# Performance work log

Hardware: AMD Instinct MI355X
Metric: run time of the kernel (lower is better)

Reference implementation:

```python
import jax, jax.numpy as jnp
import numpy as np

WEIGHT = 1.0  # init kwarg 'weight'


def _histc(x, bins):
    """torch.histc semantics: bins over [x.min(), x.max()], rightmost bin inclusive."""
    mn, mx = x.min(), x.max()
    w = (mx - mn) / bins
    safe_w = jnp.where(w > 0, w, 1.0)
    b = jnp.clip(jnp.floor((x - mn) / safe_w), 0, bins - 1).astype(jnp.int32)
    return jnp.zeros((bins,), jnp.float32).at[b].add(1.0)


def setup_inputs() -> dict:
    key = jax.random.key(0)
    k1, k2, k3 = jax.random.split(key, 3)
    C, H, W = 64, 128, 128
    inp = jax.random.normal(k1, (1, C, H, W), jnp.float32)
    match = jax.random.normal(k2, (1, C, H, W), jnp.float32)
    mask_tight = (jax.random.uniform(k3, (1, 1, H, W)) > 0.3).astype(jnp.float32)
    return {"input": inp, "match": match, "mask_tight": mask_tight, "bins": 256}


def reference(input, match, mask_tight, bins):
    C = input.shape[1]
    # --- compute_histogram (torch.histc per channel of masked match) ---
    mm = (match * mask_tight).reshape(C, -1)
    style_his = jax.lax.stop_gradient(jax.vmap(lambda v: _histc(v, bins))(mm))  # (C, bins)

    # --- remap_histogram ---
    x = (input * mask_tight).reshape(C, -1)  # (C, N)
    N = x.shape[1]
    channel_min = x.min(1, keepdims=True)  # (C,1)
    channel_max = x.max(1, keepdims=True)  # (C,1)
    step = (channel_max - channel_min) / bins
    rng = jnp.arange(1, N + 1, dtype=x.dtype)[None, :]  # (1, N) ranks 1..N

    sh = style_his * N / style_his.sum(1, keepdims=True)
    cdf = jnp.cumsum(sh, axis=1)                                  # (C, bins)
    cdf_prev = jnp.concatenate([jnp.zeros((C, 1), cdf.dtype), cdf[:, :-1]], axis=1)

    # CDF inversion: count bins whose cdf < rank  -> idx in [0, bins]
    idx = jnp.sum(cdf[:, None, :] - rng[:, :, None] < 0, axis=2).astype(jnp.int32)  # (C, N)

    # Faithful select_idx: gather from FLATTENED hist with un-offset bin indices
    flat_idx = idx.reshape(-1)
    sel = lambda h: h.reshape(-1)[flat_idx].reshape(C, N)

    ratio = jnp.clip((rng - sel(cdf_prev)) / (1e-8 + sel(cdf)), 0.0, 1.0)  # (C, N)
    input_corr = channel_min + (ratio + idx) * step
    input_corr = input_corr.at[:, -1].set(channel_max[:, 0])
    input_corr = sel(input_corr)  # faithful final flattened re-gather

    # --- loss (scalar stored as self.loss in the torch module) ---
    loss = jnp.mean((input_corr - x) ** 2)
    loss = loss * mask_tight.sum() * C / input.size * WEIGHT
    return loss
```

## Files before the change

kernel.cpp:

```cpp
#include <hip/hip_runtime.h>
#include <math.h>

#define C_CH   64
#define HW     16384
#define BINS   256
#define SPLIT  8
#define SEG    (HW / SPLIT)
#define NTHR   256

#define WS_ENC_MIN 0
#define WS_ENC_MAX 65
#define WS_SSE     130
#define WS_MASKSUM 131
#define WS_CDF     192
#define WS_T       (WS_CDF + C_CH * BINS)

__device__ inline unsigned int encf(float f) {
    unsigned int u = __float_as_uint(f);
    return (u & 0x80000000u) ? ~u : (u | 0x80000000u);
}
__device__ inline float decf(unsigned int e) {
    unsigned int u = (e & 0x80000000u) ? (e ^ 0x80000000u) : ~e;
    return __uint_as_float(u);
}

__global__ __launch_bounds__(NTHR) void k1_minmax(const float* __restrict__ input,
                                                  const float* __restrict__ match,
                                                  const float* __restrict__ mask,
                                                  unsigned int* __restrict__ ws) {
    const int c   = blockIdx.x >> 3;
    const int s   = blockIdx.x & (SPLIT - 1);
    const int tid = threadIdx.x;
    const int base = s * SEG;

    const float* m = match + c * HW + base;
    const float* mk = mask + base;

    float mn = INFINITY, mx = -INFINITY;
    #pragma unroll
    for (int k = 0; k < SEG / NTHR; k++) {
        float v = m[tid + k * NTHR] * mk[tid + k * NTHR];
        mn = fminf(mn, v);
        mx = fmaxf(mx, v);
    }

    __shared__ float red[NTHR];
    red[tid] = mn; __syncthreads();
    for (int st = 128; st > 0; st >>= 1) { if (tid < st) red[tid] = fminf(red[tid], red[tid + st]); __syncthreads(); }
    if (tid == 0) atomicMin(&ws[WS_ENC_MIN + c], encf(red[0]));
    __syncthreads();
    red[tid] = mx; __syncthreads();
    for (int st = 128; st > 0; st >>= 1) { if (tid < st) red[tid] = fmaxf(red[tid], red[tid + st]); __syncthreads(); }
    if (tid == 0) atomicMax(&ws[WS_ENC_MAX + c], encf(red[0]));

    if (c == 0) {
        const float* x = input + base;
        float xmn = INFINITY, xmx = -INFINITY, msum = 0.0f;
        #pragma unroll
        for (int k = 0; k < SEG / NTHR; k++) {
            float mv = mk[tid + k * NTHR];
            float v = x[tid + k * NTHR] * mv;
            xmn = fminf(xmn, v);
            xmx = fmaxf(xmx, v);
            msum += mv;
        }
        __syncthreads();
        red[tid] = xmn; __syncthreads();
        for (int st = 128; st > 0; st >>= 1) { if (tid < st) red[tid] = fminf(red[tid], red[tid + st]); __syncthreads(); }
        if (tid == 0) atomicMin(&ws[WS_ENC_MIN + C_CH], encf(red[0]));
        __syncthreads();
        red[tid] = xmx; __syncthreads();
        for (int st = 128; st > 0; st >>= 1) { if (tid < st) red[tid] = fmaxf(red[tid], red[tid + st]); __syncthreads(); }
        if (tid == 0) atomicMax(&ws[WS_ENC_MAX + C_CH], encf(red[0]));
        __syncthreads();
        red[tid] = msum; __syncthreads();
        for (int st = 128; st > 0; st >>= 1) { if (tid < st) red[tid] += red[tid + st]; __syncthreads(); }
        if (tid == 0) atomicAdd((float*)&ws[WS_MASKSUM], red[0]);
    }
}

__global__ __launch_bounds__(1024) void k2_hist(const float* __restrict__ match,
                                                const float* __restrict__ mask,
                                                unsigned int* __restrict__ ws) {
    const int c   = blockIdx.x;
    const int tid = threadIdx.x;
    const float* m = match + c * HW;
    float* wsf = (float*)ws;

    const float mn = decf(ws[WS_ENC_MIN + c]);
    const float mx = decf(ws[WS_ENC_MAX + c]);
    float w  = (mx - mn) * (1.0f / 256.0f);
    float sw = (w > 0.0f) ? w : 1.0f;

    __shared__ int hist[BINS];
    if (tid < BINS) hist[tid] = 0;
    __syncthreads();

    #pragma unroll
    for (int k = 0; k < HW / 1024; k++) {
        int i = tid + k * 1024;
        float v = m[i] * mask[i];
        float b = floorf((v - mn) / sw);
        b = fminf(fmaxf(b, 0.0f), 255.0f);
        atomicAdd(&hist[(int)b], 1);
    }
    __syncthreads();

    for (int off = 1; off < BINS; off <<= 1) {
        int v = 0;
        if (tid < BINS) v = hist[tid] + ((tid >= off) ? hist[tid - off] : 0);
        __syncthreads();
        if (tid < BINS) hist[tid] = v;
        __syncthreads();
    }

    if (tid < BINS) wsf[WS_CDF + c * BINS + tid] = (float)hist[tid];

    if (c == 0 && tid < BINS) {
        const float xmn = decf(ws[WS_ENC_MIN + C_CH]);
        const float xmx = decf(ws[WS_ENC_MAX + C_CH]);
        float step = (xmx - xmn) * (1.0f / 256.0f);
        float rank = (float)(tid + 1);
        int idx = 0;
        #pragma unroll 8
        for (int b = 0; b < BINS; b++) idx += (hist[b] < (tid + 1)) ? 1 : 0;
        float cp = (idx > 0) ? (float)hist[idx - 1] : 0.0f;
        float cc = (float)hist[idx];
        float ratio = (rank - cp) / (1e-8f + cc);
        ratio = fminf(fmaxf(ratio, 0.0f), 1.0f);
        wsf[WS_T + tid] = xmn + (ratio + (float)idx) * step;
    }
}

__global__ __launch_bounds__(NTHR) void k3_loss(const float* __restrict__ input,
                                                const float* __restrict__ mask,
                                                unsigned int* __restrict__ ws) {
    const int c   = blockIdx.x >> 3;
    const int s   = blockIdx.x & (SPLIT - 1);
    const int tid = threadIdx.x;
    const int base = s * SEG;
    const float* wsf = (const float*)ws;

    __shared__ float scdf[BINS];
    __shared__ float sT[BINS];
    if (tid < BINS) {
        scdf[tid] = wsf[WS_CDF + c * BINS + tid];
        sT[tid]   = wsf[WS_T + tid];
    }
    __syncthreads();

    const float* x  = input + c * HW + base;
    const float* mk = mask + base;

    int n0 = base + tid;
    float rank0 = (float)(n0 + 1);
    int lo = 0, hi = BINS;
    while (lo < hi) {
        int mid = (lo + hi) >> 1;
        if (scdf[mid] < rank0) lo = mid + 1; else hi = mid;
    }

    float acc = 0.0f;
    #pragma unroll
    for (int k = 0; k < SEG / NTHR; k++) {
        int i = tid + k * NTHR;
        float rank = (float)(base + i + 1);
        while (scdf[lo] < rank) lo++;
        float corr = sT[lo];
        float xv = x[i] * mk[i];
        float d = corr - xv;
        acc += d * d;
    }

    __shared__ float red[NTHR];
    red[tid] = acc; __syncthreads();
    for (int st = 128; st > 0; st >>= 1) { if (tid < st) red[tid] += red[tid + st]; __syncthreads(); }
    if (tid == 0) atomicAdd((float*)&ws[WS_SSE], red[0]);
}

__global__ void k4_final(const unsigned int* __restrict__ ws, float* __restrict__ out) {
    if (threadIdx.x == 0) {
        const float* wsf = (const float*)ws;
        double sse = (double)wsf[WS_SSE];
        double msum = (double)wsf[WS_MASKSUM];
        double mean = sse / (double)(C_CH * HW);
        out[0] = (float)(mean * msum * (double)C_CH / (double)(C_CH * HW));
    }
}

extern "C" void kernel_launch(void* const* d_in, const int* in_sizes, int n_in,
                              void* d_out, int out_size, void* d_ws, size_t ws_size,
                              hipStream_t stream) {
    const float* input = (const float*)d_in[0];
    const float* match = (const float*)d_in[1];
    const float* mask  = (const float*)d_in[2];
    unsigned int* ws   = (unsigned int*)d_ws;
    float* out         = (float*)d_out;

    hipMemsetAsync(ws + WS_ENC_MIN, 0xFF, 65 * sizeof(unsigned int), stream);
    hipMemsetAsync(ws + WS_ENC_MAX, 0x00, (132 - WS_ENC_MAX) * sizeof(unsigned int), stream);

    k1_minmax<<<C_CH * SPLIT, NTHR, 0, stream>>>(input, match, mask, ws);
    k2_hist  <<<C_CH, 1024, 0, stream>>>(match, mask, ws);
    k3_loss  <<<C_CH * SPLIT, NTHR, 0, stream>>>(input, mask, ws);
    k4_final <<<1, 64, 0, stream>>>(ws, out);
}
```

Measured before the change: 96.66 us.

## Fuse all stages into one cooperative kernel with grid syncs

Replaces the two memsets and four kernel launches with a single cooperative kernel that uses grid-wide syncs between the min/max, histogram, CDF/remap and loss phases. Per-block partials written to workspace replace the global atomics. The histogram is split across 8 blocks per channel, and loads are vectorized to float4. This removes launch and memset overhead and keeps more blocks busy during histogramming, at the cost of grid.sync latency and each block redundantly rescanning the channel-0 histogram.

```diff
diff --git a/kernel.cpp b/kernel.cpp
--- a/kernel.cpp
+++ b/kernel.cpp
@@ -1,5 +1,8 @@
 #include <hip/hip_runtime.h>
+#include <hip/hip_cooperative_groups.h>
 #include <math.h>
+
+namespace cg = cooperative_groups;
 
 #define C_CH   64
 #define HW     16384
@@ -7,184 +10,198 @@
 #define SPLIT  8
 #define SEG    (HW / SPLIT)
 #define NTHR   256
-
-#define WS_ENC_MIN 0
-#define WS_ENC_MAX 65
-#define WS_SSE     130
-#define WS_MASKSUM 131
-#define WS_CDF     192
-#define WS_T       (WS_CDF + C_CH * BINS)
-
-__device__ inline unsigned int encf(float f) {
-    unsigned int u = __float_as_uint(f);
-    return (u & 0x80000000u) ? ~u : (u | 0x80000000u);
-}
-__device__ inline float decf(unsigned int e) {
-    unsigned int u = (e & 0x80000000u) ? (e ^ 0x80000000u) : ~e;
-    return __uint_as_float(u);
-}
-
-__global__ __launch_bounds__(NTHR) void k1_minmax(const float* __restrict__ input,
-                                                  const float* __restrict__ match,
-                                                  const float* __restrict__ mask,
-                                                  unsigned int* __restrict__ ws) {
-    const int c   = blockIdx.x >> 3;
-    const int s   = blockIdx.x & (SPLIT - 1);
-    const int tid = threadIdx.x;
+#define NBLK   (C_CH * SPLIT)
+
+#define WS_PMN   0
+#define WS_PMX   512
+#define WS_PXMN  1024
+#define WS_PXMX  1032
+#define WS_PMS   1040
+#define WS_SSE   1048
+#define WS_HIST8 2048
+
+__device__ inline float4 ld4(const float* p) { return *(const float4*)p; }
+
+__device__ inline int lbound(const float* a, float rank) {
+    int lo = 0, hi = BINS;
+    while (lo < hi) { int mid = (lo + hi) >> 1; if (a[mid] < rank) lo = mid + 1; else hi = mid; }
+    return (lo > 255) ? 255 : lo;
+}
+
+__device__ inline void scan256(int* h, int tid) {
+    for (int off = 1; off < BINS; off <<= 1) {
+        int v = h[tid] + ((tid >= off) ? h[tid - off] : 0);
+        __syncthreads();
+        h[tid] = v;
+        __syncthreads();
+    }
+}
+
+__device__ inline float blk_reduce(float v, float* red, int tid, bool is_min, bool is_max) {
+    red[tid] = v; __syncthreads();
+    for (int st = 128; st > 0; st >>= 1) {
+        if (tid < st) {
+            float a = red[tid], b = red[tid + st];
+            red[tid] = is_min ? fminf(a, b) : (is_max ? fmaxf(a, b) : (a + b));
+        }
+        __syncthreads();
+    }
+    float r = red[0]; __syncthreads();
+    return r;
+}
+
+__global__ __launch_bounds__(NTHR, 2) void fused(const float* __restrict__ input,
+                                                 const float* __restrict__ match,
+                                                 const float* __restrict__ mask,
+                                                 float* ws, float* out) {
+    cg::grid_group grid = cg::this_grid();
+    const int b = blockIdx.x, c = b >> 3, s = b & (SPLIT - 1), tid = threadIdx.x;
     const int base = s * SEG;
-
-    const float* m = match + c * HW + base;
+    int* wsi = (int*)ws;
+
+    __shared__ float red[NTHR];
+    __shared__ int   ihist[BINS];
+    __shared__ float scdf[BINS];
+    __shared__ float sT[BINS];
+
+    const float* m  = match + c * HW + base;
     const float* mk = mask + base;
-
-    float mn = INFINITY, mx = -INFINITY;
-    #pragma unroll
-    for (int k = 0; k < SEG / NTHR; k++) {
-        float v = m[tid + k * NTHR] * mk[tid + k * NTHR];
-        mn = fminf(mn, v);
-        mx = fmaxf(mx, v);
-    }
-
-    __shared__ float red[NTHR];
-    red[tid] = mn; __syncthreads();
-    for (int st = 128; st > 0; st >>= 1) { if (tid < st) red[tid] = fminf(red[tid], red[tid + st]); __syncthreads(); }
-    if (tid == 0) atomicMin(&ws[WS_ENC_MIN + c], encf(red[0]));
-    __syncthreads();
-    red[tid] = mx; __syncthreads();
-    for (int st = 128; st > 0; st >>= 1) { if (tid < st) red[tid] = fmaxf(red[tid], red[tid + st]); __syncthreads(); }
-    if (tid == 0) atomicMax(&ws[WS_ENC_MAX + c], encf(red[0]));
-
-    if (c == 0) {
-        const float* x = input + base;
-        float xmn = INFINITY, xmx = -INFINITY, msum = 0.0f;
-        #pragma unroll
-        for (int k = 0; k < SEG / NTHR; k++) {
-            float mv = mk[tid + k * NTHR];
-            float v = x[tid + k * NTHR] * mv;
-            xmn = fminf(xmn, v);
-            xmx = fmaxf(xmx, v);
-            msum += mv;
-        }
-        __syncthreads();
-        red[tid] = xmn; __syncthreads();
-        for (int st = 128; st > 0; st >>= 1) { if (tid < st) red[tid] = fminf(red[tid], red[tid + st]); __syncthreads(); }
-        if (tid == 0) atomicMin(&ws[WS_ENC_MIN + C_CH], encf(red[0]));
-        __syncthreads();
-        red[tid] = xmx; __syncthreads();
-        for (int st = 128; st > 0; st >>= 1) { if (tid < st) red[tid] = fmaxf(red[tid], red[tid + st]); __syncthreads(); }
-        if (tid == 0) atomicMax(&ws[WS_ENC_MAX + C_CH], encf(red[0]));
-        __syncthreads();
-        red[tid] = msum; __syncthreads();
-        for (int st = 128; st > 0; st >>= 1) { if (tid < st) red[tid] += red[tid + st]; __syncthreads(); }
-        if (tid == 0) atomicAdd((float*)&ws[WS_MASKSUM], red[0]);
-    }
-}
-
-__global__ __launch_bounds__(1024) void k2_hist(const float* __restrict__ match,
-                                                const float* __restrict__ mask,
-                                                unsigned int* __restrict__ ws) {
-    const int c   = blockIdx.x;
-    const int tid = threadIdx.x;
-    const float* m = match + c * HW;
-    float* wsf = (float*)ws;
-
-    const float mn = decf(ws[WS_ENC_MIN + c]);
-    const float mx = decf(ws[WS_ENC_MAX + c]);
-    float w  = (mx - mn) * (1.0f / 256.0f);
-    float sw = (w > 0.0f) ? w : 1.0f;
-
-    __shared__ int hist[BINS];
-    if (tid < BINS) hist[tid] = 0;
-    __syncthreads();
-
-    #pragma unroll
-    for (int k = 0; k < HW / 1024; k++) {
-        int i = tid + k * 1024;
-        float v = m[i] * mask[i];
-        float b = floorf((v - mn) / sw);
-        b = fminf(fmaxf(b, 0.0f), 255.0f);
-        atomicAdd(&hist[(int)b], 1);
-    }
-    __syncthreads();
-
-    for (int off = 1; off < BINS; off <<= 1) {
-        int v = 0;
-        if (tid < BINS) v = hist[tid] + ((tid >= off) ? hist[tid - off] : 0);
-        __syncthreads();
-        if (tid < BINS) hist[tid] = v;
-        __syncthreads();
-    }
-
-    if (tid < BINS) wsf[WS_CDF + c * BINS + tid] = (float)hist[tid];
-
-    if (c == 0 && tid < BINS) {
-        const float xmn = decf(ws[WS_ENC_MIN + C_CH]);
-        const float xmx = decf(ws[WS_ENC_MAX + C_CH]);
+    const float* x  = input + c * HW + base;
+
+    {
+        float mn = INFINITY, mx = -INFINITY;
+        #pragma unroll
+        for (int k = 0; k < 2; k++) {
+            float4 mv = ld4(m + k * 1024 + 4 * tid);
+            float4 kv = ld4(mk + k * 1024 + 4 * tid);
+            float v0 = mv.x * kv.x, v1 = mv.y * kv.y, v2 = mv.z * kv.z, v3 = mv.w * kv.w;
+            mn = fminf(mn, fminf(fminf(v0, v1), fminf(v2, v3)));
+            mx = fmaxf(mx, fmaxf(fmaxf(v0, v1), fmaxf(v2, v3)));
+        }
+        mn = blk_reduce(mn, red, tid, true, false);
+        mx = blk_reduce(mx, red, tid, false, true);
+        if (tid == 0) { ws[WS_PMN + b] = mn; ws[WS_PMX + b] = mx; }
+
+        if (c == 0) {
+            float xmn = INFINITY, xmx = -INFINITY, msum = 0.0f;
+            #pragma unroll
+            for (int k = 0; k < 2; k++) {
+                float4 xv = ld4(x + k * 1024 + 4 * tid);
+                float4 kv = ld4(mk + k * 1024 + 4 * tid);
+                float v0 = xv.x * kv.x, v1 = xv.y * kv.y, v2 = xv.z * kv.z, v3 = xv.w * kv.w;
+                xmn = fminf(xmn, fminf(fminf(v0, v1), fminf(v2, v3)));
+                xmx = fmaxf(xmx, fmaxf(fmaxf(v0, v1), fmaxf(v2, v3)));
+                msum += kv.x + kv.y + kv.z + kv.w;
+            }
+            xmn = blk_reduce(xmn, red, tid, true, false);
+            xmx = blk_reduce(xmx, red, tid, false, true);
+            msum = blk_reduce(msum, red, tid, false, false);
+            if (tid == 0) { ws[WS_PXMN + s] = xmn; ws[WS_PXMX + s] = xmx; ws[WS_PMS + s] = msum; }
+        }
+    }
+    __threadfence();
+    grid.sync();
+
+    {
+        float mn = INFINITY, mx = -INFINITY;
+        #pragma unroll
+        for (int j = 0; j < SPLIT; j++) {
+            mn = fminf(mn, ws[WS_PMN + c * SPLIT + j]);
+            mx = fmaxf(mx, ws[WS_PMX + c * SPLIT + j]);
+        }
+        float w  = (mx - mn) * (1.0f / 256.0f);
+        float sw = (w > 0.0f) ? w : 1.0f;
+
+        ihist[tid] = 0;
+        __syncthreads();
+        #pragma unroll
+        for (int k = 0; k < 2; k++) {
+            float4 mv = ld4(m + k * 1024 + 4 * tid);
+            float4 kv = ld4(mk + k * 1024 + 4 * tid);
+            float v[4] = { mv.x * kv.x, mv.y * kv.y, mv.z * kv.z, mv.w * kv.w };
+            #pragma unroll
+            for (int j = 0; j < 4; j++) {
+                float bb = floorf((v[j] - mn) / sw);
+                bb = fminf(fmaxf(bb, 0.0f), 255.0f);
+                atomicAdd(&ihist[(int)bb], 1);
+            }
+        }
+        __syncthreads();
+        wsi[WS_HIST8 + b * BINS + tid] = ihist[tid];
+    }
+    __threadfence();
+    grid.sync();
+
+    {
+        int h = 0;
+        #pragma unroll
+        for (int j = 0; j < SPLIT; j++) h += wsi[WS_HIST8 + (c * SPLIT + j) * BINS + tid];
+        ihist[tid] = h;
+        __syncthreads();
+        scan256(ihist, tid);
+        scdf[tid] = (float)ihist[tid];
+        __syncthreads();
+
+        if (c != 0) {
+            int h0 = 0;
+            #pragma unroll
+            for (int j = 0; j < SPLIT; j++) h0 += wsi[WS_HIST8 + j * BINS + tid];
+            ihist[tid] = h0;
+            __syncthreads();
+            scan256(ihist, tid);
+        }
+        red[tid] = (float)ihist[tid];
+        __syncthreads();
+
+        float xmn = INFINITY, xmx = -INFINITY;
+        #pragma unroll
+        for (int j = 0; j < SPLIT; j++) {
+            xmn = fminf(xmn, ws[WS_PXMN + j]);
+            xmx = fmaxf(xmx, ws[WS_PXMX + j]);
+        }
         float step = (xmx - xmn) * (1.0f / 256.0f);
         float rank = (float)(tid + 1);
-        int idx = 0;
-        #pragma unroll 8
-        for (int b = 0; b < BINS; b++) idx += (hist[b] < (tid + 1)) ? 1 : 0;
-        float cp = (idx > 0) ? (float)hist[idx - 1] : 0.0f;
-        float cc = (float)hist[idx];
-        float ratio = (rank - cp) / (1e-8f + cc);
-        ratio = fminf(fmaxf(ratio, 0.0f), 1.0f);
-        wsf[WS_T + tid] = xmn + (ratio + (float)idx) * step;
-    }
-}
-
-__global__ __launch_bounds__(NTHR) void k3_loss(const float* __restrict__ input,
-                                                const float* __restrict__ mask,
-                                                unsigned int* __restrict__ ws) {
-    const int c   = blockIdx.x >> 3;
-    const int s   = blockIdx.x & (SPLIT - 1);
-    const int tid = threadIdx.x;
-    const int base = s * SEG;
-    const float* wsf = (const float*)ws;
-
-    __shared__ float scdf[BINS];
-    __shared__ float sT[BINS];
-    if (tid < BINS) {
-        scdf[tid] = wsf[WS_CDF + c * BINS + tid];
-        sT[tid]   = wsf[WS_T + tid];
-    }
-    __syncthreads();
-
-    const float* x  = input + c * HW + base;
-    const float* mk = mask + base;
-
-    int n0 = base + tid;
-    float rank0 = (float)(n0 + 1);
-    int lo = 0, hi = BINS;
-    while (lo < hi) {
-        int mid = (lo + hi) >> 1;
-        if (scdf[mid] < rank0) lo = mid + 1; else hi = mid;
-    }
-
-    float acc = 0.0f;
-    #pragma unroll
-    for (int k = 0; k < SEG / NTHR; k++) {
-        int i = tid + k * NTHR;
-        float rank = (float)(base + i + 1);
-        while (scdf[lo] < rank) lo++;
-        float corr = sT[lo];
-        float xv = x[i] * mk[i];
-        float d = corr - xv;
-        acc += d * d;
-    }
-
-    __shared__ float red[NTHR];
-    red[tid] = acc; __syncthreads();
-    for (int st = 128; st > 0; st >>= 1) { if (tid < st) red[tid] += red[tid + st]; __syncthreads(); }
-    if (tid == 0) atomicAdd((float*)&ws[WS_SSE], red[0]);
-}
-
-__global__ void k4_final(const unsigned int* __restrict__ ws, float* __restrict__ out) {
-    if (threadIdx.x == 0) {
-        const float* wsf = (const float*)ws;
-        double sse = (double)wsf[WS_SSE];
-        double msum = (double)wsf[WS_MASKSUM];
-        double mean = sse / (double)(C_CH * HW);
-        out[0] = (float)(mean * msum * (double)C_CH / (double)(C_CH * HW));
+        int idx = lbound(red, rank);
+        float cp = (idx > 0) ? red[idx - 1] : 0.0f;
+        float cc = red[idx];
+        float ratio = fminf(fmaxf((rank - cp) / (1e-8f + cc), 0.0f), 1.0f);
+        sT[tid] = xmn + (ratio + (float)idx) * step;
+        __syncthreads();
+
+        float rank0 = (float)(base + 4 * tid + 1);
+        int lo = lbound(scdf, rank0);
+
+        float acc = 0.0f;
+        #pragma unroll
+        for (int k = 0; k < 2; k++) {
+            float4 xv = ld4(x + k * 1024 + 4 * tid);
+            float4 kv = ld4(mk + k * 1024 + 4 * tid);
+            float v[4] = { xv.x * kv.x, xv.y * kv.y, xv.z * kv.z, xv.w * kv.w };
+            int n0 = base + k * 1024 + 4 * tid;
+            #pragma unroll
+            for (int j = 0; j < 4; j++) {
+                float rnk = (float)(n0 + j + 1);
+                while (scdf[lo] < rnk) lo++;
+                float d = sT[lo] - v[j];
+                acc += d * d;
+            }
+        }
+        acc = blk_reduce(acc, red, tid, false, false);
+        if (tid == 0) ws[WS_SSE + b] = acc;
+    }
+    __threadfence();
+    grid.sync();
+
+    if (b == 0) {
+        float v = ws[WS_SSE + tid] + ws[WS_SSE + NTHR + tid];
+        float sse = blk_reduce(v, red, tid, false, false);
+        if (tid == 0) {
+            float msum = 0.0f;
+            #pragma unroll
+            for (int j = 0; j < SPLIT; j++) msum += ws[WS_PMS + j];
+            double mean = (double)sse / (double)(C_CH * HW);
+            out[0] = (float)(mean * (double)msum * (double)C_CH / (double)(C_CH * HW));
+        }
     }
 }
 
@@ -194,14 +211,9 @@
     const float* input = (const float*)d_in[0];
     const float* match = (const float*)d_in[1];
     const float* mask  = (const float*)d_in[2];
-    unsigned int* ws   = (unsigned int*)d_ws;
+    float* ws          = (float*)d_ws;
     float* out         = (float*)d_out;
 
-    hipMemsetAsync(ws + WS_ENC_MIN, 0xFF, 65 * sizeof(unsigned int), stream);
-    hipMemsetAsync(ws + WS_ENC_MAX, 0x00, (132 - WS_ENC_MAX) * sizeof(unsigned int), stream);
-
-    k1_minmax<<<C_CH * SPLIT, NTHR, 0, stream>>>(input, match, mask, ws);
-    k2_hist  <<<C_CH, 1024, 0, stream>>>(match, mask, ws);
-    k3_loss  <<<C_CH * SPLIT, NTHR, 0, stream>>>(input, mask, ws);
-    k4_final <<<1, 64, 0, stream>>>(ws, out);
-}
+    void* args[] = { (void*)&input, (void*)&match, (void*)&mask, (void*)&ws, (void*)&out };
+    hipLaunchCooperativeKernel((const void*)fused, dim3(NBLK), dim3(NTHR), args, 0, stream);
+}
```

Result: slower. 358.6 us (+271.0%).
